# Kernel optimization log

Hardware: AMD Instinct MI355X
Metric: run time of the kernel (lower is better)

The kernel has to match this reference:

```python
import jax, jax.numpy as jnp
import numpy as np
from functools import partial

# Module hyperparameters (from init_kwargs)
T, C_IN, H, W_DIM = 128, 16, 64, 64
C_OUT, KH, KW = 64, 3, 3
PAD = ((1, 1), (1, 1))  # (top,bottom),(left,right) -> symmetric here
STRIDES = (1, 1)
F_V_THRESH = 8.0
F_V_THRESH_LOW = -1.0
F_V_RESET = 0.0
# fVSubtract is None -> reset-to-value branch


def setup_inputs() -> dict:
    key = jax.random.key(0)
    kx, kw, kb = jax.random.split(key, 3)
    x = jax.random.uniform(kx, (T, C_IN, H, W_DIM), dtype=jnp.float32)
    fan_in = C_IN * KH * KW
    bound = 1.0 / np.sqrt(fan_in)
    W = jax.random.uniform(kw, (C_OUT, C_IN, KH, KW), dtype=jnp.float32,
                           minval=-bound, maxval=bound)
    b = jax.random.uniform(kb, (C_OUT,), dtype=jnp.float32,
                           minval=-bound, maxval=bound)
    return {"x": x, "W": W, "b": b}


def _spiking_conv(x, W, b):
    # conv over all timesteps at once (time is the conv batch dim): [T, C_out, H, W]
    conv_out = jax.lax.conv_general_dilated(
        x, W, window_strides=STRIDES, padding=PAD,
        dimension_numbers=("NCHW", "OIHW", "NCHW"))
    conv_out = conv_out + b[None, :, None, None]

    def step(state, conv_t):
        state = state + conv_t
        spikes = (state >= F_V_THRESH).astype(conv_t.dtype)
        # reset-to-value branch (fVSubtract is None)
        state = spikes * F_V_RESET + state * (1.0 - spikes)
        # nn.Threshold(v, v): x if x > v else v
        state = jnp.where(state > F_V_THRESH_LOW, state, F_V_THRESH_LOW)
        return state, spikes

    init_state = jnp.zeros(conv_out.shape[1:], dtype=conv_out.dtype)
    _, num_spikes = jax.lax.scan(step, init_state, conv_out)
    return num_spikes  # [T, C_out, H, W] float (0/1)


def reference(x, W, b):
    return _spiking_conv(x, W, b)
```

## Files before the change

### kernel.cpp

```cpp
#include <hip/hip_runtime.h>

#define T_STEPS 128
#define CIN     16
#define HH      64
#define WW      64
#define COUT    64
#define HWSZ    (HH * WW)
#define CHW     (COUT * HWSZ)
#define XCHW    (CIN * HWSZ)

#define TILE    32
#define HALO    34
#define LSTR    36
#define PLANE   (HALO * LSTR)
#define NSTAGE  (CIN * HALO * HALO)

__global__ __launch_bounds__(512, 4)
void spiking_conv_pass1(const float* __restrict__ x, const float* __restrict__ Wt,
                        const float* __restrict__ b, float* __restrict__ out) {
    __shared__ float xs[CIN * PLANE];

    const int tid = threadIdx.x;
    const int t   = blockIdx.y;
    const int h0  = (blockIdx.x >> 1) * TILE;
    const int w0  = (blockIdx.x & 1) * TILE;

    const float* xt = x + t * XCHW;
    for (int e = tid; e < NSTAGE; e += 512) {
        int ci  = e / (HALO * HALO);
        int rem = e - ci * (HALO * HALO);
        int r   = rem / HALO;
        int c   = rem - r * HALO;
        int gh  = h0 - 1 + r;
        int gw  = w0 - 1 + c;
        float v = 0.f;
        if ((unsigned)gh < HH && (unsigned)gw < WW)
            v = xt[ci * HWSZ + gh * WW + gw];
        xs[ci * PLANE + r * LSTR + c] = v;
    }
    __syncthreads();

    const int pr0 = tid >> 4;
    const int pc0 = (tid & 15) * 2;
    float* outt = out + t * CHW;

#pragma unroll 1
    for (int cog = 0; cog < 8; ++cog) {
        float acc[8][2];
#pragma unroll
        for (int j = 0; j < 8; ++j) { acc[j][0] = 0.f; acc[j][1] = 0.f; }

#pragma unroll 1
        for (int ci = 0; ci < CIN; ++ci) {
            float w[72];
#pragma unroll
            for (int j = 0; j < 8; ++j)
#pragma unroll
                for (int k = 0; k < 9; ++k)
                    w[j * 9 + k] = Wt[(cog * 8 + j) * (CIN * 9) + ci * 9 + k];

            float xv[3][4];
#pragma unroll
            for (int dr = 0; dr < 3; ++dr) {
                const float* row = &xs[ci * PLANE + (pr0 + dr) * LSTR + pc0];
                float2 a = *(const float2*)row;
                float2 c2 = *(const float2*)(row + 2);
                xv[dr][0] = a.x; xv[dr][1] = a.y;
                xv[dr][2] = c2.x; xv[dr][3] = c2.y;
            }

#pragma unroll
            for (int j = 0; j < 8; ++j)
#pragma unroll
                for (int ky = 0; ky < 3; ++ky)
#pragma unroll
                    for (int kx = 0; kx < 3; ++kx) {
                        const float wv = w[j * 9 + ky * 3 + kx];
                        acc[j][0] += wv * xv[ky][kx];
                        acc[j][1] += wv * xv[ky][kx + 1];
                    }
        }

#pragma unroll
        for (int j = 0; j < 8; ++j) {
            const float bias = b[cog * 8 + j];
            float2 o;
            o.x = acc[j][0] + bias;
            o.y = acc[j][1] + bias;
            *(float2*)&outt[(cog * 8 + j) * HWSZ + (h0 + pr0) * WW + (w0 + pc0)] = o;
        }
    }
}

__global__ __launch_bounds__(256)
void spiking_scan_pass2(float* __restrict__ io) {
    const int idx = blockIdx.x * 256 + threadIdx.x;
    float* p = io + idx;
    float s = 0.f;
#pragma unroll 1
    for (int tb = 0; tb < T_STEPS / 8; ++tb) {
        float v[8];
#pragma unroll
        for (int i = 0; i < 8; ++i) v[i] = p[(tb * 8 + i) * CHW];
#pragma unroll
        for (int i = 0; i < 8; ++i) {
            s += v[i];
            const bool sp = (s >= 8.0f);
            v[i] = sp ? 1.0f : 0.0f;
            s = sp ? 0.0f : s;
            s = fmaxf(s, -1.0f);
        }
#pragma unroll
        for (int i = 0; i < 8; ++i) p[(tb * 8 + i) * CHW] = v[i];
    }
}

extern "C" void kernel_launch(void* const* d_in, const int* in_sizes, int n_in,
                              void* d_out, int out_size, void* d_ws, size_t ws_size,
                              hipStream_t stream) {
    const float* x = (const float*)d_in[0];
    const float* W = (const float*)d_in[1];
    const float* b = (const float*)d_in[2];
    float* out = (float*)d_out;

    dim3 g1(4, 128);
    spiking_conv_pass1<<<g1, 512, 0, stream>>>(x, W, b, out);

    spiking_scan_pass2<<<CHW / 256, 256, 0, stream>>>(out);
}
```

Before: 292.7 us.

## Split conv output channels across grid z, batch input channels, prefetch scan loads

The conv kernel now launches two blocks per tile and timestep, each computing 32 output channels, which doubles the block count and so the parallelism. The inner loop processes four input channels at once and loads weights as float4 through an opaque zero offset so they come from vector memory rather than scalar loads. The staging loop is fully unrolled with bounds guards. The scan kernel software-pipelines its loads, fetching the next 8 timesteps while the current ones are processed. The cost is that the input halo is staged twice, once per channel half, and register pressure in the conv kernel rises.

```diff
diff --git a/kernel.cpp b/kernel.cpp
--- a/kernel.cpp
+++ b/kernel.cpp
@@ -24,9 +24,16 @@
     const int t   = blockIdx.y;
     const int h0  = (blockIdx.x >> 1) * TILE;
     const int w0  = (blockIdx.x & 1) * TILE;
+    const int co0 = blockIdx.z * 32;
+
+    int vz;
+    asm volatile("v_mov_b32 %0, 0" : "=v"(vz));
 
     const float* xt = x + t * XCHW;
-    for (int e = tid; e < NSTAGE; e += 512) {
+#pragma unroll
+    for (int k = 0; k < 37; ++k) {
+        int e = tid + k * 512;
+        bool ok = (e < NSTAGE);
         int ci  = e / (HALO * HALO);
         int rem = e - ci * (HALO * HALO);
         int r   = rem / HALO;
@@ -34,9 +41,9 @@
         int gh  = h0 - 1 + r;
         int gw  = w0 - 1 + c;
         float v = 0.f;
-        if ((unsigned)gh < HH && (unsigned)gw < WW)
+        if (ok && (unsigned)gh < HH && (unsigned)gw < WW)
             v = xt[ci * HWSZ + gh * WW + gw];
-        xs[ci * PLANE + r * LSTR + c] = v;
+        if (ok) xs[ci * PLANE + r * LSTR + c] = v;
     }
     __syncthreads();
 
@@ -45,49 +52,58 @@
     float* outt = out + t * CHW;
 
 #pragma unroll 1
-    for (int cog = 0; cog < 8; ++cog) {
+    for (int cog = 0; cog < 4; ++cog) {
         float acc[8][2];
 #pragma unroll
         for (int j = 0; j < 8; ++j) { acc[j][0] = 0.f; acc[j][1] = 0.f; }
 
 #pragma unroll 1
-        for (int ci = 0; ci < CIN; ++ci) {
-            float w[72];
+        for (int cib = 0; cib < 4; ++cib) {
+            float xv[4][3][4];
 #pragma unroll
-            for (int j = 0; j < 8; ++j)
+            for (int ci4 = 0; ci4 < 4; ++ci4) {
+                const int ci = cib * 4 + ci4;
 #pragma unroll
-                for (int k = 0; k < 9; ++k)
-                    w[j * 9 + k] = Wt[(cog * 8 + j) * (CIN * 9) + ci * 9 + k];
-
-            float xv[3][4];
+                for (int dr = 0; dr < 3; ++dr) {
+                    const float* row = &xs[ci * PLANE + (pr0 + dr) * LSTR + pc0];
+                    float2 a  = *(const float2*)row;
+                    float2 c2 = *(const float2*)(row + 2);
+                    xv[ci4][dr][0] = a.x;  xv[ci4][dr][1] = a.y;
+                    xv[ci4][dr][2] = c2.x; xv[ci4][dr][3] = c2.y;
+                }
+            }
 #pragma unroll
-            for (int dr = 0; dr < 3; ++dr) {
-                const float* row = &xs[ci * PLANE + (pr0 + dr) * LSTR + pc0];
-                float2 a = *(const float2*)row;
-                float2 c2 = *(const float2*)(row + 2);
-                xv[dr][0] = a.x; xv[dr][1] = a.y;
-                xv[dr][2] = c2.x; xv[dr][3] = c2.y;
+            for (int j = 0; j < 8; ++j) {
+                const int co = co0 + cog * 8 + j;
+                const float* wb = Wt + co * (CIN * 9) + cib * 36 + vz;
+                float w[36];
+#pragma unroll
+                for (int q = 0; q < 9; ++q) {
+                    float4 f = *(const float4*)(wb + q * 4);
+                    w[q * 4 + 0] = f.x; w[q * 4 + 1] = f.y;
+                    w[q * 4 + 2] = f.z; w[q * 4 + 3] = f.w;
+                }
+#pragma unroll
+                for (int ci4 = 0; ci4 < 4; ++ci4)
+#pragma unroll
+                    for (int ky = 0; ky < 3; ++ky)
+#pragma unroll
+                        for (int kx = 0; kx < 3; ++kx) {
+                            const float wv = w[ci4 * 9 + ky * 3 + kx];
+                            acc[j][0] += wv * xv[ci4][ky][kx];
+                            acc[j][1] += wv * xv[ci4][ky][kx + 1];
+                        }
             }
-
-#pragma unroll
-            for (int j = 0; j < 8; ++j)
-#pragma unroll
-                for (int ky = 0; ky < 3; ++ky)
-#pragma unroll
-                    for (int kx = 0; kx < 3; ++kx) {
-                        const float wv = w[j * 9 + ky * 3 + kx];
-                        acc[j][0] += wv * xv[ky][kx];
-                        acc[j][1] += wv * xv[ky][kx + 1];
-                    }
         }
 
 #pragma unroll
         for (int j = 0; j < 8; ++j) {
-            const float bias = b[cog * 8 + j];
+            const int co = co0 + cog * 8 + j;
+            const float bias = b[co];
             float2 o;
             o.x = acc[j][0] + bias;
             o.y = acc[j][1] + bias;
-            *(float2*)&outt[(cog * 8 + j) * HWSZ + (h0 + pr0) * WW + (w0 + pc0)] = o;
+            *(float2*)&outt[co * HWSZ + (h0 + pr0) * WW + (w0 + pc0)] = o;
         }
     }
 }
@@ -97,21 +113,34 @@
     const int idx = blockIdx.x * 256 + threadIdx.x;
     float* p = io + idx;
     float s = 0.f;
+    float v[8], nv[8];
+#pragma unroll
+    for (int i = 0; i < 8; ++i) v[i] = p[i * CHW];
 #pragma unroll 1
-    for (int tb = 0; tb < T_STEPS / 8; ++tb) {
-        float v[8];
+    for (int tb = 0; tb < 15; ++tb) {
 #pragma unroll
-        for (int i = 0; i < 8; ++i) v[i] = p[(tb * 8 + i) * CHW];
+        for (int i = 0; i < 8; ++i) nv[i] = p[((tb + 1) * 8 + i) * CHW];
+        float o[8];
 #pragma unroll
         for (int i = 0; i < 8; ++i) {
             s += v[i];
             const bool sp = (s >= 8.0f);
-            v[i] = sp ? 1.0f : 0.0f;
+            o[i] = sp ? 1.0f : 0.0f;
             s = sp ? 0.0f : s;
             s = fmaxf(s, -1.0f);
         }
 #pragma unroll
-        for (int i = 0; i < 8; ++i) p[(tb * 8 + i) * CHW] = v[i];
+        for (int i = 0; i < 8; ++i) p[(tb * 8 + i) * CHW] = o[i];
+#pragma unroll
+        for (int i = 0; i < 8; ++i) v[i] = nv[i];
+    }
+#pragma unroll
+    for (int i = 0; i < 8; ++i) {
+        s += v[i];
+        const bool sp = (s >= 8.0f);
+        p[(120 + i) * CHW] = sp ? 1.0f : 0.0f;
+        s = sp ? 0.0f : s;
+        s = fmaxf(s, -1.0f);
     }
 }
 
@@ -123,7 +152,7 @@
     const float* b = (const float*)d_in[2];
     float* out = (float*)d_out;
 
-    dim3 g1(4, 128);
+    dim3 g1(4, 128, 2);
     spiking_conv_pass1<<<g1, 512, 0, stream>>>(x, W, b, out);
 
     spiking_scan_pass2<<<CHW / 256, 256, 0, stream>>>(out);
```

Measured after the change: 476.2 us. +62.7%, slower.

## Retile conv by output-channel quarters with wider register blocking and vectorize scan

Applied to the files above, without the earlier changes.

The conv kernel now assigns each block a half-image by 16 output channels. It stages the input in two 8-channel chunks and computes 4 pixels by 16 channels per thread, which raises register reuse of weights and inputs. The scan pass processes two pixels per thread with nontemporal loads and stores and batches 32 timesteps per iteration. Register pressure rises sharply with 64 accumulators plus 72 weights under launch_bounds(512,4), which may cause spills.

```diff
diff --git a/kernel.cpp b/kernel.cpp
--- a/kernel.cpp
+++ b/kernel.cpp
@@ -9,109 +9,134 @@
 #define CHW     (COUT * HWSZ)
 #define XCHW    (CIN * HWSZ)
 
-#define TILE    32
-#define HALO    34
-#define LSTR    36
-#define PLANE   (HALO * LSTR)
-#define NSTAGE  (CIN * HALO * HALO)
+#define TR      34
+#define TC      66
+#define LSTR    68
+#define PLANE   (TR * LSTR)
+#define NST     (8 * TR * TC)
 
 __global__ __launch_bounds__(512, 4)
 void spiking_conv_pass1(const float* __restrict__ x, const float* __restrict__ Wt,
                         const float* __restrict__ b, float* __restrict__ out) {
-    __shared__ float xs[CIN * PLANE];
+    __shared__ float xs[8 * PLANE];
 
-    const int tid = threadIdx.x;
-    const int t   = blockIdx.y;
-    const int h0  = (blockIdx.x >> 1) * TILE;
-    const int w0  = (blockIdx.x & 1) * TILE;
+    const int tid  = threadIdx.x;
+    const int t    = blockIdx.y;
+    const int half = blockIdx.x & 1;
+    const int coq  = blockIdx.x >> 1;
+    const int h0   = half * 32;
+    const int co0  = coq * 16;
 
-    const float* xt = x + t * XCHW;
-    for (int e = tid; e < NSTAGE; e += 512) {
-        int ci  = e / (HALO * HALO);
-        int rem = e - ci * (HALO * HALO);
-        int r   = rem / HALO;
-        int c   = rem - r * HALO;
-        int gh  = h0 - 1 + r;
-        int gw  = w0 - 1 + c;
-        float v = 0.f;
-        if ((unsigned)gh < HH && (unsigned)gw < WW)
-            v = xt[ci * HWSZ + gh * WW + gw];
-        xs[ci * PLANE + r * LSTR + c] = v;
-    }
-    __syncthreads();
+    const float* xt  = x + t * XCHW;
+    float* outt      = out + t * CHW;
+    const int pr0 = tid >> 4;
+    const int pc0 = (tid & 15) * 4;
 
-    const int pr0 = tid >> 4;
-    const int pc0 = (tid & 15) * 2;
-    float* outt = out + t * CHW;
+    float acc[2][8][4];
+#pragma unroll
+    for (int g = 0; g < 2; ++g)
+#pragma unroll
+        for (int j = 0; j < 8; ++j)
+#pragma unroll
+            for (int p = 0; p < 4; ++p) acc[g][j][p] = 0.f;
 
 #pragma unroll 1
-    for (int cog = 0; cog < 8; ++cog) {
-        float acc[8][2];
-#pragma unroll
-        for (int j = 0; j < 8; ++j) { acc[j][0] = 0.f; acc[j][1] = 0.f; }
+    for (int chunk = 0; chunk < 2; ++chunk) {
+        if (chunk) __syncthreads();
+        for (int e = tid; e < NST; e += 512) {
+            int ci  = e / (TR * TC);
+            int rem = e - ci * (TR * TC);
+            int r   = rem / TC;
+            int c   = rem - r * TC;
+            int gh  = h0 - 1 + r;
+            int gw  = c - 1;
+            float v = 0.f;
+            if ((unsigned)gh < HH && (unsigned)gw < WW)
+                v = xt[(chunk * 8 + ci) * HWSZ + gh * WW + gw];
+            xs[ci * PLANE + r * LSTR + c] = v;
+        }
+        __syncthreads();
 
 #pragma unroll 1
-        for (int ci = 0; ci < CIN; ++ci) {
-            float w[72];
-#pragma unroll
-            for (int j = 0; j < 8; ++j)
-#pragma unroll
-                for (int k = 0; k < 9; ++k)
-                    w[j * 9 + k] = Wt[(cog * 8 + j) * (CIN * 9) + ci * 9 + k];
-
-            float xv[3][4];
+        for (int ci = 0; ci < 8; ++ci) {
+            float xv[3][6];
 #pragma unroll
             for (int dr = 0; dr < 3; ++dr) {
                 const float* row = &xs[ci * PLANE + (pr0 + dr) * LSTR + pc0];
-                float2 a = *(const float2*)row;
-                float2 c2 = *(const float2*)(row + 2);
-                xv[dr][0] = a.x; xv[dr][1] = a.y;
-                xv[dr][2] = c2.x; xv[dr][3] = c2.y;
+                float4 a  = *(const float4*)row;
+                float2 c2 = *(const float2*)(row + 4);
+                xv[dr][0] = a.x;  xv[dr][1] = a.y;
+                xv[dr][2] = a.z;  xv[dr][3] = a.w;
+                xv[dr][4] = c2.x; xv[dr][5] = c2.y;
             }
+#pragma unroll
+            for (int cog = 0; cog < 2; ++cog) {
+                float w[72];
+#pragma unroll
+                for (int j = 0; j < 8; ++j)
+#pragma unroll
+                    for (int k = 0; k < 9; ++k)
+                        w[j * 9 + k] = Wt[(co0 + cog * 8 + j) * (CIN * 9) +
+                                          (chunk * 8 + ci) * 9 + k];
+#pragma unroll
+                for (int j = 0; j < 8; ++j)
+#pragma unroll
+                    for (int ky = 0; ky < 3; ++ky)
+#pragma unroll
+                        for (int kx = 0; kx < 3; ++kx) {
+                            const float wv = w[j * 9 + ky * 3 + kx];
+#pragma unroll
+                            for (int p = 0; p < 4; ++p)
+                                acc[cog][j][p] += wv * xv[ky][kx + p];
+                        }
+            }
+        }
+    }
 
 #pragma unroll
-            for (int j = 0; j < 8; ++j)
-#pragma unroll
-                for (int ky = 0; ky < 3; ++ky)
-#pragma unroll
-                    for (int kx = 0; kx < 3; ++kx) {
-                        const float wv = w[j * 9 + ky * 3 + kx];
-                        acc[j][0] += wv * xv[ky][kx];
-                        acc[j][1] += wv * xv[ky][kx + 1];
-                    }
-        }
-
+    for (int cog = 0; cog < 2; ++cog)
 #pragma unroll
         for (int j = 0; j < 8; ++j) {
-            const float bias = b[cog * 8 + j];
-            float2 o;
-            o.x = acc[j][0] + bias;
-            o.y = acc[j][1] + bias;
-            *(float2*)&outt[(cog * 8 + j) * HWSZ + (h0 + pr0) * WW + (w0 + pc0)] = o;
+            const int co = co0 + cog * 8 + j;
+            const float bias = b[co];
+            float4 o;
+            o.x = acc[cog][j][0] + bias;
+            o.y = acc[cog][j][1] + bias;
+            o.z = acc[cog][j][2] + bias;
+            o.w = acc[cog][j][3] + bias;
+            *(float4*)&outt[co * HWSZ + (h0 + pr0) * WW + pc0] = o;
         }
-    }
 }
+
+typedef float v2f __attribute__((ext_vector_type(2)));
 
 __global__ __launch_bounds__(256)
 void spiking_scan_pass2(float* __restrict__ io) {
     const int idx = blockIdx.x * 256 + threadIdx.x;
-    float* p = io + idx;
-    float s = 0.f;
+    v2f* p = (v2f*)io + idx;
+    float sx = 0.f, sy = 0.f;
 #pragma unroll 1
-    for (int tb = 0; tb < T_STEPS / 8; ++tb) {
-        float v[8];
+    for (int tb = 0; tb < 4; ++tb) {
+        v2f v[32];
 #pragma unroll
-        for (int i = 0; i < 8; ++i) v[i] = p[(tb * 8 + i) * CHW];
+        for (int i = 0; i < 32; ++i)
+            v[i] = __builtin_nontemporal_load(&p[(size_t)(tb * 32 + i) * (CHW / 2)]);
 #pragma unroll
-        for (int i = 0; i < 8; ++i) {
-            s += v[i];
-            const bool sp = (s >= 8.0f);
-            v[i] = sp ? 1.0f : 0.0f;
-            s = sp ? 0.0f : s;
-            s = fmaxf(s, -1.0f);
+        for (int i = 0; i < 32; ++i) {
+            sx += v[i].x;
+            bool spx = (sx >= 8.0f);
+            v[i].x = spx ? 1.0f : 0.0f;
+            sx = spx ? 0.0f : sx;
+            sx = fmaxf(sx, -1.0f);
+            sy += v[i].y;
+            bool spy = (sy >= 8.0f);
+            v[i].y = spy ? 1.0f : 0.0f;
+            sy = spy ? 0.0f : sy;
+            sy = fmaxf(sy, -1.0f);
         }
 #pragma unroll
-        for (int i = 0; i < 8; ++i) p[(tb * 8 + i) * CHW] = v[i];
+        for (int i = 0; i < 32; ++i)
+            __builtin_nontemporal_store(v[i], &p[(size_t)(tb * 32 + i) * (CHW / 2)]);
     }
 }
 
@@ -123,8 +148,8 @@
     const float* b = (const float*)d_in[2];
     float* out = (float*)d_out;
 
-    dim3 g1(4, 128);
+    dim3 g1(8, 128);
     spiking_conv_pass1<<<g1, 512, 0, stream>>>(x, W, b, out);
 
-    spiking_scan_pass2<<<CHW / 256, 256, 0, stream>>>(out);
+    spiking_scan_pass2<<<(CHW / 2) / 256, 256, 0, stream>>>(out);
 }
```

After: 336.0 us. 1.15x slower.

## Split conv across output-channel groups, widen per-thread tile, pipeline scan loads

Applied to the files above, without the earlier changes.

Adds a small kernel that repacks weights into contiguous per-group blocks so each warp reads uniform, contiguous weights. The conv kernel gains a grid z dimension of 4 output-channel quarters, and each half of the 512 threads handles 8 channels with 4 pixels per thread instead of looping over 8 channel groups. This raises block count and FMA reuse of loaded inputs, at the cost of restaging the input halo four times. The scan kernel now processes 16 timesteps per chunk and prefetches the next chunk before computing, to overlap memory latency.

```diff
diff --git a/kernel.cpp b/kernel.cpp
--- a/kernel.cpp
+++ b/kernel.cpp
@@ -13,10 +13,22 @@
 #define HALO    34
 #define LSTR    36
 #define PLANE   (HALO * LSTR)
-#define NSTAGE  (CIN * HALO * HALO)
+#define NST     (CIN * HALO * HALO)
+#define WBLK    80
+
+__global__ void transpose_w(const float* __restrict__ W, float* __restrict__ Wtr) {
+    int e = blockIdx.x * 256 + threadIdx.x;
+    if (e >= COUT * CIN * 9) return;
+    int co = e / (CIN * 9);
+    int r  = e - co * (CIN * 9);
+    int ci = r / 9;
+    int k  = r - ci * 9;
+    int coq = co >> 4, cog = (co >> 3) & 1, j = co & 7;
+    Wtr[(((coq * 2 + cog) * CIN) + ci) * WBLK + j * 9 + k] = W[e];
+}
 
 __global__ __launch_bounds__(512, 4)
-void spiking_conv_pass1(const float* __restrict__ x, const float* __restrict__ Wt,
+void spiking_conv_pass1(const float* __restrict__ x, const float* __restrict__ Wtr,
                         const float* __restrict__ b, float* __restrict__ out) {
     __shared__ float xs[CIN * PLANE];
 
@@ -24,9 +36,10 @@
     const int t   = blockIdx.y;
     const int h0  = (blockIdx.x >> 1) * TILE;
     const int w0  = (blockIdx.x & 1) * TILE;
+    const int coq = blockIdx.z;
 
     const float* xt = x + t * XCHW;
-    for (int e = tid; e < NSTAGE; e += 512) {
+    for (int e = tid; e < NST; e += 512) {
         int ci  = e / (HALO * HALO);
         int rem = e - ci * (HALO * HALO);
         int r   = rem / HALO;
@@ -40,55 +53,63 @@
     }
     __syncthreads();
 
-    const int pr0 = tid >> 4;
-    const int pc0 = (tid & 15) * 2;
+    const int cog = __builtin_amdgcn_readfirstlane(tid >> 8);
+    const int sp  = tid & 255;
+    const int pr0 = sp >> 3;
+    const int pc0 = (sp & 7) * 4;
+    const float* wbase = Wtr + (coq * 2 + cog) * (CIN * WBLK);
     float* outt = out + t * CHW;
 
-#pragma unroll 1
-    for (int cog = 0; cog < 8; ++cog) {
-        float acc[8][2];
+    float acc[8][4];
 #pragma unroll
-        for (int j = 0; j < 8; ++j) { acc[j][0] = 0.f; acc[j][1] = 0.f; }
+    for (int j = 0; j < 8; ++j)
+#pragma unroll
+        for (int p = 0; p < 4; ++p) acc[j][p] = 0.f;
 
 #pragma unroll 1
-        for (int ci = 0; ci < CIN; ++ci) {
-            float w[72];
+    for (int ci = 0; ci < CIN; ++ci) {
+        float xv[3][6];
 #pragma unroll
-            for (int j = 0; j < 8; ++j)
+        for (int dr = 0; dr < 3; ++dr) {
+            const float* row = &xs[ci * PLANE + (pr0 + dr) * LSTR + pc0];
+            float4 a  = *(const float4*)row;
+            float2 c2 = *(const float2*)(row + 4);
+            xv[dr][0] = a.x;  xv[dr][1] = a.y;
+            xv[dr][2] = a.z;  xv[dr][3] = a.w;
+            xv[dr][4] = c2.x; xv[dr][5] = c2.y;
+        }
 #pragma unroll
-                for (int k = 0; k < 9; ++k)
-                    w[j * 9 + k] = Wt[(cog * 8 + j) * (CIN * 9) + ci * 9 + k];
-
-            float xv[3][4];
+        for (int half = 0; half < 2; ++half) {
+            float w[36];
 #pragma unroll
-            for (int dr = 0; dr < 3; ++dr) {
-                const float* row = &xs[ci * PLANE + (pr0 + dr) * LSTR + pc0];
-                float2 a = *(const float2*)row;
-                float2 c2 = *(const float2*)(row + 2);
-                xv[dr][0] = a.x; xv[dr][1] = a.y;
-                xv[dr][2] = c2.x; xv[dr][3] = c2.y;
-            }
-
+            for (int i = 0; i < 36; ++i)
+                w[i] = wbase[ci * WBLK + half * 36 + i];
 #pragma unroll
-            for (int j = 0; j < 8; ++j)
+            for (int jj = 0; jj < 4; ++jj) {
+                const int j = half * 4 + jj;
 #pragma unroll
                 for (int ky = 0; ky < 3; ++ky)
 #pragma unroll
                     for (int kx = 0; kx < 3; ++kx) {
-                        const float wv = w[j * 9 + ky * 3 + kx];
-                        acc[j][0] += wv * xv[ky][kx];
-                        acc[j][1] += wv * xv[ky][kx + 1];
+                        const float wv = w[jj * 9 + ky * 3 + kx];
+#pragma unroll
+                        for (int p = 0; p < 4; ++p)
+                            acc[j][p] += wv * xv[ky][kx + p];
                     }
+            }
         }
+    }
 
 #pragma unroll
-        for (int j = 0; j < 8; ++j) {
-            const float bias = b[cog * 8 + j];
-            float2 o;
-            o.x = acc[j][0] + bias;
-            o.y = acc[j][1] + bias;
-            *(float2*)&outt[(cog * 8 + j) * HWSZ + (h0 + pr0) * WW + (w0 + pc0)] = o;
-        }
+    for (int j = 0; j < 8; ++j) {
+        const int co = coq * 16 + cog * 8 + j;
+        const float bias = b[co];
+        float4 o;
+        o.x = acc[j][0] + bias;
+        o.y = acc[j][1] + bias;
+        o.z = acc[j][2] + bias;
+        o.w = acc[j][3] + bias;
+        *(float4*)&outt[co * HWSZ + (h0 + pr0) * WW + (w0 + pc0)] = o;
     }
 }
 
@@ -97,21 +118,34 @@
     const int idx = blockIdx.x * 256 + threadIdx.x;
     float* p = io + idx;
     float s = 0.f;
+    float v[16], nv[16];
+#pragma unroll
+    for (int i = 0; i < 16; ++i) v[i] = p[i * CHW];
 #pragma unroll 1
-    for (int tb = 0; tb < T_STEPS / 8; ++tb) {
-        float v[8];
+    for (int tb = 0; tb < 7; ++tb) {
 #pragma unroll
-        for (int i = 0; i < 8; ++i) v[i] = p[(tb * 8 + i) * CHW];
+        for (int i = 0; i < 16; ++i) nv[i] = p[((tb + 1) * 16 + i) * CHW];
+        float o[16];
 #pragma unroll
-        for (int i = 0; i < 8; ++i) {
+        for (int i = 0; i < 16; ++i) {
             s += v[i];
             const bool sp = (s >= 8.0f);
-            v[i] = sp ? 1.0f : 0.0f;
+            o[i] = sp ? 1.0f : 0.0f;
             s = sp ? 0.0f : s;
             s = fmaxf(s, -1.0f);
         }
 #pragma unroll
-        for (int i = 0; i < 8; ++i) p[(tb * 8 + i) * CHW] = v[i];
+        for (int i = 0; i < 16; ++i) p[(tb * 16 + i) * CHW] = o[i];
+#pragma unroll
+        for (int i = 0; i < 16; ++i) v[i] = nv[i];
+    }
+#pragma unroll
+    for (int i = 0; i < 16; ++i) {
+        s += v[i];
+        const bool sp = (s >= 8.0f);
+        p[(112 + i) * CHW] = sp ? 1.0f : 0.0f;
+        s = sp ? 0.0f : s;
+        s = fmaxf(s, -1.0f);
     }
 }
 
@@ -122,9 +156,12 @@
     const float* W = (const float*)d_in[1];
     const float* b = (const float*)d_in[2];
     float* out = (float*)d_out;
+    float* Wtr = (float*)d_ws;
 
-    dim3 g1(4, 128);
-    spiking_conv_pass1<<<g1, 512, 0, stream>>>(x, W, b, out);
+    transpose_w<<<36, 256, 0, stream>>>(W, Wtr);
+
+    dim3 g1(4, 128, 4);
+    spiking_conv_pass1<<<g1, 512, 0, stream>>>(x, Wtr, b, out);
 
     spiking_scan_pass2<<<CHW / 256, 256, 0, stream>>>(out);
 }
```

After: 309.1 us. 1.06x slower.
